# Kernel optimization log

Hardware: AMD Instinct MI355X
Metric: run time of the kernel (lower is better)

The kernel has to match this reference:

```python
import jax, jax.numpy as jnp
import numpy as np

C_CURV = 0.01
K = 20
BALL_EPS = 4e-3  # hyptorch float32 boundary eps


def _e2p(x, c=C_CURV):
    # ToPoincare: expmap0 then project onto the Poincare ball
    sqrt_c = c ** 0.5
    n = jnp.maximum(jnp.linalg.norm(x, axis=-1, keepdims=True), 1e-15)
    y = jnp.tanh(sqrt_c * n) * x / (sqrt_c * n)
    maxnorm = (1.0 - BALL_EPS) / sqrt_c
    ny = jnp.maximum(jnp.linalg.norm(y, axis=-1, keepdims=True), 1e-15)
    return jnp.where(ny > maxnorm, y * (maxnorm / ny), y)


def _mobius_add(x, y, c=C_CURV):
    x2 = jnp.sum(x * x, axis=-1, keepdims=True)
    y2 = jnp.sum(y * y, axis=-1, keepdims=True)
    xy = jnp.sum(x * y, axis=-1, keepdims=True)
    num = (1.0 + 2.0 * c * xy + c * y2) * x + (1.0 - c * x2) * y
    den = 1.0 + 2.0 * c * xy + c * c * x2 * y2
    return num / jnp.maximum(den, 1e-15)


def _knn(x, k):
    # x: (B, C, N); Euclidean negative squared distance, topk indices
    inner = -2.0 * jnp.einsum('bcn,bcm->bnm', x, x)
    xx = jnp.sum(x * x, axis=1)  # (B, N)
    pd = -xx[:, :, None] - inner - xx[:, None, :]
    return jax.lax.top_k(pd, k)[1]  # (B, N, k)


def _graph_feature(x, k=K):
    # x: (B, C, N) -> (B, 2C, N, k)
    idx = _knn(x, k)
    xp = _e2p(jnp.transpose(x, (0, 2, 1)))  # (B, N, C) on Poincare ball
    feat = jax.vmap(lambda xb, ib: xb[ib])(xp, idx)  # (B, N, k, C) gather
    xc = jnp.broadcast_to(xp[:, :, None, :], feat.shape)
    out = jnp.concatenate([_mobius_add(feat, -xc), xc], axis=-1)
    return jnp.transpose(out, (0, 3, 1, 2))


def _bn(x, g, b, axes, eps=1e-5):
    # BatchNorm (training-mode batch statistics), channel axis = 1
    m = jnp.mean(x, axis=axes, keepdims=True)
    v = jnp.mean((x - m) ** 2, axis=axes, keepdims=True)
    shp = [1] * x.ndim
    shp[1] = -1
    return (x - m) / jnp.sqrt(v + eps) * g.reshape(shp) + b.reshape(shp)


def _ln(x, g, b, eps=1e-5):
    m = jnp.mean(x, axis=-1, keepdims=True)
    v = jnp.mean((x - m) ** 2, axis=-1, keepdims=True)
    return (x - m) / jnp.sqrt(v + eps) * g + b


def setup_inputs() -> dict:
    key = jax.random.key(0)
    ks = jax.random.split(key, 8)
    B, N, OUT = 16, 1024, 40
    s = 0.05
    return {
        'x': jax.random.normal(ks[0], (B, N, 3), jnp.float32),
        'conv1_w': jax.random.normal(ks[1], (64, 6), jnp.float32) * s,
        'bn1_g': jnp.ones((64,), jnp.float32), 'bn1_b': jnp.zeros((64,), jnp.float32),
        'conv2_w': jax.random.normal(ks[2], (192, 128), jnp.float32) * s,
        'bn2_g': jnp.ones((192,), jnp.float32), 'bn2_b': jnp.zeros((192,), jnp.float32),
        'conv3_w': jax.random.normal(ks[3], (1024, 256), jnp.float32) * s,
        'bn3_g': jnp.ones((1024,), jnp.float32), 'bn3_b': jnp.zeros((1024,), jnp.float32),
        'fc1_w': jax.random.normal(ks[4], (512, 1024), jnp.float32) * s,
        'fc1_b': jnp.zeros((512,), jnp.float32),
        'ln1_g': jnp.ones((512,), jnp.float32), 'ln1_b': jnp.zeros((512,), jnp.float32),
        'fc2_w': jax.random.normal(ks[5], (256, 512), jnp.float32) * s,
        'fc2_b': jnp.zeros((256,), jnp.float32),
        'ln2_g': jnp.ones((256,), jnp.float32), 'ln2_b': jnp.zeros((256,), jnp.float32),
        'out_w': jax.random.normal(ks[6], (OUT, 256), jnp.float32) * s,
        'out_b': jnp.zeros((OUT,), jnp.float32),
    }


def reference(x, conv1_w, bn1_g, bn1_b, conv2_w, bn2_g, bn2_b,
              conv3_w, bn3_g, bn3_b, fc1_w, fc1_b, ln1_g, ln1_b,
              fc2_w, fc2_b, ln2_g, ln2_b, out_w, out_b):
    xt = jnp.transpose(x, (0, 2, 1))  # (B, 3, N)
    f = _graph_feature(xt)            # (B, 6, N, k)
    h = jnp.einsum('oc,bcnk->bonk', conv1_w, f)
    h = jax.nn.relu(_bn(h, bn1_g, bn1_b, (0, 2, 3)))
    x1 = jnp.max(h, axis=-1)          # (B, 64, N)
    f = _graph_feature(x1)            # (B, 128, N, k)
    h = jnp.einsum('oc,bcnk->bonk', conv2_w, f)
    h = jax.nn.relu(_bn(h, bn2_g, bn2_b, (0, 2, 3)))
    x2 = jnp.max(h, axis=-1)          # (B, 192, N)
    h = jnp.concatenate([x1, x2], axis=1)  # (B, 256, N)
    h = jnp.einsum('oc,bcn->bon', conv3_w, h)
    h = jax.nn.relu(_bn(h, bn3_g, bn3_b, (0, 2)))
    h = jnp.max(h, axis=-1)           # (B, 1024)
    h = jax.nn.relu(_ln(h @ fc1_w.T + fc1_b, ln1_g, ln1_b))
    h = jax.nn.relu(_ln(h @ fc2_w.T + fc2_b, ln2_g, ln2_b))
    logits = h @ out_w.T + out_b      # (B, outdim)
    return jax.nn.log_softmax(logits, axis=1)
```

## Files before the change

kernel.cpp:

```cpp
#include <hip/hip_runtime.h>
#include <math.h>

#define B_ 16
#define N_ 1024
#define KNN 20
#define NPAIR (B_*N_)

typedef __attribute__((ext_vector_type(8))) short bf16x8;
typedef __attribute__((ext_vector_type(4))) float f32x4;

__device__ __forceinline__ unsigned fkey(float f) {
  unsigned u = __float_as_uint(f);
  return (u & 0x80000000u) ? ~u : (u | 0x80000000u);
}
__device__ __forceinline__ float fkeyinv(unsigned u) {
  unsigned b = (u & 0x80000000u) ? (u ^ 0x80000000u) : ~u;
  return __uint_as_float(b);
}
__device__ __forceinline__ unsigned short f2bf(float x) {
  unsigned u = __float_as_uint(x);
  unsigned r = (u + 0x7FFFu + ((u >> 16) & 1u)) >> 16;
  return (unsigned short)r;
}
__device__ __forceinline__ float bf2f(unsigned short u) {
  return __uint_as_float(((unsigned)u) << 16);
}
__device__ __forceinline__ unsigned short f2h(float x) {
  _Float16 h = (_Float16)x;
  return *(unsigned short*)&h;
}
__device__ __forceinline__ float h2f(unsigned short u) {
  _Float16 h = *(_Float16*)&u;
  return (float)h;
}
__device__ __forceinline__ unsigned knnkey(float d, int idx) {
  return (fkey(d) & 0xFFFFFC00u) | (unsigned)(1023 - idx);
}

__device__ __forceinline__ void topk_insert_u32(unsigned (&kl)[KNN], unsigned nk) {
  kl[KNN-1] = nk;
  #pragma unroll
  for (int i = KNN-1; i > 0; i--) {
    unsigned hi = max(kl[i-1], kl[i]);
    unsigned lo = min(kl[i-1], kl[i]);
    kl[i-1] = hi; kl[i] = lo;
  }
}

__device__ __forceinline__ int cnt_gt(const unsigned* __restrict__ L, unsigned v) {
  int j = 0;
  #pragma unroll
  for (int s = 16; s; s >>= 1) {
    int nj = j + s;
    if (nj <= KNN && L[nj-1] > v) j = nj;
  }
  return j;
}

__global__ void __launch_bounds__(256) k_prep_knn1(const float* __restrict__ x,
        float* __restrict__ xp1, const float* __restrict__ w2, const float* __restrict__ w3,
        unsigned short* __restrict__ w2h, unsigned short* __restrict__ wt3h,
        unsigned* __restrict__ keypart) {
  __shared__ float P[N_*3];
  __shared__ float XX[N_];
  if (blockIdx.x >= 512) {
    int i = (blockIdx.x - 512) * 256 + threadIdx.x;
    if (i < NPAIR) {
      float a0 = x[i*3+0], a1 = x[i*3+1], a2 = x[i*3+2];
      float n = sqrtf(a0*a0 + a1*a1 + a2*a2);
      n = fmaxf(n, 1e-15f);
      float th = tanhf(0.1f * n);
      float sc = th / (0.1f * n);
      float ny = fmaxf(th * 10.0f, 1e-15f);
      float mxn = (1.0f - 4e-3f) / 0.1f;
      if (ny > mxn) sc *= mxn / ny;
      xp1[i*3+0] = sc*a0; xp1[i*3+1] = sc*a1; xp1[i*3+2] = sc*a2;
    }
    if (i < 192*128) w2h[i] = f2bf(w2[i]);
    wt3h[i] = f2bf(w3[i]);
    return;
  }
  int blk = blockIdx.x;
  int b = blk >> 5, rc = (blk >> 3) & 3, cc = blk & 7;
  const float* xb = x + b*N_*3;
  for (int e = threadIdx.x; e < N_*3; e += 256) P[e] = xb[e];
  __syncthreads();
  for (int j = threadIdx.x; j < N_; j += 256) {
    float q0 = P[j*3], q1 = P[j*3+1], q2 = P[j*3+2];
    XX[j] = q0*q0 + q1*q1 + q2*q2;
  }
  __syncthreads();
  int r = rc*256 + threadIdx.x;
  float q0 = P[r*3], q1 = P[r*3+1], q2 = P[r*3+2];
  float xxq = XX[r];
  unsigned kl[KNN];
  #pragma unroll
  for (int i = 0; i < KNN; i++) kl[i] = 0u;
  int cbase = cc*128;
  for (int jj = 0; jj < 128; jj++) {
    int j = cbase + jj;
    float dot = q0*P[j*3] + q1*P[j*3+1] + q2*P[j*3+2];
    float d = 2.0f*dot - xxq - XX[j];
    unsigned nk = knnkey(d, j);
    if (nk > kl[KNN-1]) topk_insert_u32(kl, nk);
  }
  int p = b*N_ + r;
  unsigned* pe = keypart + (size_t)p*160 + cc*20;
  #pragma unroll
  for (int i = 0; i < KNN; i++) pe[i] = kl[i];
}

__global__ void __launch_bounds__(256) k_conv1(const float* __restrict__ xp1,
                        const unsigned* __restrict__ keypart,
                        const float* __restrict__ w1, float* __restrict__ hmax1,
                        float* __restrict__ hmin1, float* __restrict__ stats1sh) {
  __shared__ float F[4][KNN][6];
  __shared__ float red[4][64][2];
  __shared__ int idxs[16][KNN];
  __shared__ unsigned keybuf[2560];
  __shared__ unsigned out1[1280];
  __shared__ unsigned out2[640];
  int g = threadIdx.x >> 6, lane = threadIdx.x & 63;
  int tid = threadIdx.x;
  int pbase = blockIdx.x * 16;
  {
    const unsigned* src = keypart + (size_t)pbase*160;
    for (int e = tid; e < 2560; e += 256) keybuf[e] = src[e];
  }
  float w[6];
  #pragma unroll
  for (int c = 0; c < 6; c++) w[c] = w1[lane*6 + c];
  __syncthreads();
  for (int e = tid; e < 2560; e += 256) {
    int pt = e / 160, rem = e - pt*160;
    int m = rem / 40, i = rem - m*40;
    const unsigned* A = keybuf + pt*160 + (2*m)*20;
    const unsigned* Bl = A + 20;
    unsigned v; const unsigned* S; int own;
    if (i < 20) { v = A[i]; S = Bl; own = i; }
    else { v = Bl[i-20]; S = A; own = i-20; }
    int rank = own + cnt_gt(S, v);
    if (rank < KNN) out1[(pt*4 + m)*20 + rank] = v;
  }
  __syncthreads();
  for (int e = tid; e < 1280; e += 256) {
    int pt = e / 80, rem = e - pt*80;
    int m2 = rem / 40, i = rem - m2*40;
    const unsigned* A = out1 + (pt*4 + 2*m2)*20;
    const unsigned* Bl = A + 20;
    unsigned v; const unsigned* S; int own;
    if (i < 20) { v = A[i]; S = Bl; own = i; }
    else { v = Bl[i-20]; S = A; own = i-20; }
    int rank = own + cnt_gt(S, v);
    if (rank < KNN) out2[(pt*2 + m2)*20 + rank] = v;
  }
  __syncthreads();
  for (int e = tid; e < 640; e += 256) {
    int pt = e / 40, i = e - pt*40;
    const unsigned* A = out2 + pt*40;
    const unsigned* Bl = A + 20;
    unsigned v; const unsigned* S; int own;
    if (i < 20) { v = A[i]; S = Bl; own = i; }
    else { v = Bl[i-20]; S = A; own = i-20; }
    int rank = own + cnt_gt(S, v);
    if (rank < KNN) idxs[pt][rank] = 1023 - (int)(v & 1023u);
  }
  float sum = 0.f, sumsq = 0.f;
  __syncthreads();
  for (int it = 0; it < 4; ++it) {
    int p = pbase + it*4 + g;
    if (lane < KNN) {
      int nb = idxs[it*4 + g][lane];
      int bb = p >> 10;
      const float* xc = xp1 + p*3;
      const float* ft = xp1 + (bb*N_ + nb)*3;
      float x0 = ft[0], x1 = ft[1], x2v = ft[2];
      float c0 = xc[0], c1 = xc[1], c2 = xc[2];
      float X2 = x0*x0 + x1*x1 + x2v*x2v;
      float Y2 = c0*c0 + c1*c1 + c2*c2;
      float XY = -(x0*c0 + x1*c1 + x2v*c2);
      float den = fmaxf(1.0f + 0.02f*XY + 1e-4f*X2*Y2, 1e-15f);
      float s1 = (1.0f + 0.02f*XY + 0.01f*Y2) / den;
      float s2 = (1.0f - 0.01f*X2) / den;
      F[g][lane][0] = s1*x0 - s2*c0;
      F[g][lane][1] = s1*x1 - s2*c1;
      F[g][lane][2] = s1*x2v - s2*c2;
      F[g][lane][3] = c0; F[g][lane][4] = c1; F[g][lane][5] = c2;
    }
    __syncthreads();
    float mx = -__builtin_inff(), mn = __builtin_inff();
    for (int k = 0; k < KNN; k++) {
      float h = 0.f;
      #pragma unroll
      for (int c = 0; c < 6; c++) h = fmaf(w[c], F[g][k][c], h);
      mx = fmaxf(mx, h); mn = fminf(mn, h);
      sum += h; sumsq += h*h;
    }
    hmax1[(pbase + it*4 + g)*64 + lane] = mx;
    hmin1[(pbase + it*4 + g)*64 + lane] = mn;
    __syncthreads();
  }
  red[g][lane][0] = sum; red[g][lane][1] = sumsq;
  __syncthreads();
  if (g == 0) {
    float s  = red[0][lane][0] + red[1][lane][0] + red[2][lane][0] + red[3][lane][0];
    float s2 = red[0][lane][1] + red[1][lane][1] + red[2][lane][1] + red[3][lane][1];
    float* dst = stats1sh + ((size_t)(blockIdx.x & 63)*64 + lane)*2;
    atomicAdd(dst, s);
    atomicAdd(dst + 1, s2);
  }
}

__global__ void __launch_bounds__(64) k_bn_reduce(const float* __restrict__ sh, int nch, int nslots,
                            double cnt,
                            const float* __restrict__ g, const float* __restrict__ bb,
                            float* __restrict__ scale, float* __restrict__ shift) {
  int o = blockIdx.x, t = threadIdx.x;
  double s = 0.0, s2 = 0.0;
  for (int sl = t; sl < nslots; sl += 64) {
    s  += (double)sh[((size_t)sl*nch + o)*2];
    s2 += (double)sh[((size_t)sl*nch + o)*2 + 1];
  }
  #pragma unroll
  for (int off = 32; off > 0; off >>= 1) { s += __shfl_xor(s, off); s2 += __shfl_xor(s2, off); }
  if (t == 0) {
    double m = s / cnt;
    double v = s2 / cnt - m*m;
    float a = g[o] / sqrtf((float)v + 1e-5f);
    scale[o] = a;
    shift[o] = bb[o] - a * (float)m;
  }
}

__global__ void __launch_bounds__(256) k_bn1_apply(const float* __restrict__ hmax1, const float* __restrict__ hmin1,
                            const float* __restrict__ scale1, const float* __restrict__ shift1,
                            float* __restrict__ xp2,
                            unsigned short* __restrict__ x1h, unsigned short* __restrict__ x1l,
                            float* __restrict__ xx1) {
  int b = blockIdx.x >> 4, nc = blockIdx.x & 15;
  int c = threadIdx.x & 63, sub = threadIdx.x >> 6;
  int n0 = nc*64 + sub*16;
  float a = scale1[c], t = shift1[c];
  #pragma unroll
  for (int i = 0; i < 16; i++) {
    int p = b*1024 + n0 + i;
    float h = (a >= 0.f) ? hmax1[(size_t)p*64 + c] : hmin1[(size_t)p*64 + c];
    float x1 = fmaxf(fmaf(a, h, t), 0.f);
    unsigned short hb = f2bf(x1);
    x1h[(size_t)p*64 + c] = hb;
    x1l[(size_t)p*64 + c] = f2bf(x1 - bf2f(hb));
    float n2 = x1*x1;
    #pragma unroll
    for (int off = 32; off > 0; off >>= 1) n2 += __shfl_xor(n2, off);
    if (c == 0) xx1[p] = n2;
    float n1 = fmaxf(sqrtf(n2), 1e-15f);
    float th = tanhf(0.1f * n1);
    float sc = th / (0.1f * n1);
    float ny = fmaxf(th * 10.0f, 1e-15f);
    float mxn = (1.0f - 4e-3f) / 0.1f;
    if (ny > mxn) sc *= mxn / ny;
    xp2[(size_t)p*64 + c] = sc * x1;
  }
}

__global__ void __launch_bounds__(256) k_knn2g(const unsigned short* __restrict__ x1h,
        const unsigned short* __restrict__ x1l,
        const float* __restrict__ xx1, unsigned* __restrict__ keypart2) {
  __shared__ __align__(16) float SM[4096];
  int tid = threadIdx.x;
  int bi = blockIdx.x;
  int blk = ((bi & 7) << 7) + (bi >> 3);
  int b = blk >> 6, qc = (blk >> 2) & 15, cc = blk & 3;
  int qbase = qc*64, ccbase = cc*256;
  int wave = tid >> 6, lane = tid & 63;
  int lm = lane & 15, kq = lane >> 4;
  const size_t base = (size_t)b * 65536;

  bf16x8 Qh[4][2], Ql[4][2];
  #pragma unroll
  for (int qt = 0; qt < 4; qt++) {
    size_t ro = base + (size_t)(qbase + qt*16 + lm)*64 + kq*8;
    #pragma unroll
    for (int ks = 0; ks < 2; ks++) {
      Qh[qt][ks] = *((const bf16x8*)(x1h + ro + ks*32));
      Ql[qt][ks] = *((const bf16x8*)(x1l + ro + ks*32));
    }
  }
  unsigned kl[KNN];
  #pragma unroll
  for (int i = 0; i < KNN; i++) kl[i] = 0u;
  int cq = lane + (lane >> 2);

  for (int st = 0; st < 4; ++st) {
    int cb0 = ccbase + st*64;
    size_t co = base + (size_t)(cb0 + wave*16 + lm)*64 + kq*8;
    bf16x8 Ah[2], Al[2];
    #pragma unroll
    for (int ks = 0; ks < 2; ks++) {
      Ah[ks] = *((const bf16x8*)(x1h + co + ks*32));
      Al[ks] = *((const bf16x8*)(x1l + co + ks*32));
    }
    float4 xxc = *((const float4*)(xx1 + b*1024 + cb0 + wave*16 + kq*4));
    f32x4 acc[4];
    #pragma unroll
    for (int qt = 0; qt < 4; qt++) acc[qt] = (f32x4){0.f, 0.f, 0.f, 0.f};
    #pragma unroll
    for (int ks = 0; ks < 2; ks++) {
      #pragma unroll
      for (int qt = 0; qt < 4; qt++) {
        acc[qt] = __builtin_amdgcn_mfma_f32_16x16x32_bf16(Ah[ks], Qh[qt][ks], acc[qt], 0, 0, 0);
        acc[qt] = __builtin_amdgcn_mfma_f32_16x16x32_bf16(Ah[ks], Ql[qt][ks], acc[qt], 0, 0, 0);
        acc[qt] = __builtin_amdgcn_mfma_f32_16x16x32_bf16(Al[ks], Qh[qt][ks], acc[qt], 0, 0, 0);
        acc[qt] = __builtin_amdgcn_mfma_f32_16x16x32_bf16(Al[ks], Ql[qt][ks], acc[qt], 0, 0, 0);
      }
    }
    __syncthreads();
    float xxcv[4] = {xxc.x, xxc.y, xxc.z, xxc.w};
    #pragma unroll
    for (int qt = 0; qt < 4; qt++) {
      int q = qt*16 + lm;
      #pragma unroll
      for (int r = 0; r < 4; r++) {
        int c = wave*16 + kq*4 + r;
        SM[q*64 + ((c + q + (q>>2)) & 63)] = 2.0f*acc[qt][r] - xxcv[r];
      }
    }
    __syncthreads();
    #pragma unroll
    for (int j = 0; j < 16; j++) {
      int c = wave*16 + j;
      float d = SM[lane*64 + ((c + cq) & 63)];
      unsigned nk = knnkey(d, cb0 + c);
      if (nk > kl[KNN-1]) topk_insert_u32(kl, nk);
    }
  }
  __syncthreads();
  unsigned* U = (unsigned*)SM;
  unsigned* L0 = U;
  unsigned* L1 = U + 1344;
  unsigned* M  = U + 2688;
  if (wave == 0) {
    #pragma unroll
    for (int i = 0; i < KNN; i++) L0[lane*21 + i] = kl[i];
  } else if (wave == 1) {
    #pragma unroll
    for (int i = 0; i < KNN; i++) L1[lane*21 + i] = kl[i];
  }
  __syncthreads();
  if (tid < 64) {
    int ia = 0, ib = 0;
    for (int t = 0; t < KNN; t++) {
      unsigned pa = L0[tid*21 + ia], pb = L1[tid*21 + ib];
      bool ta = pa > pb;
      M[tid*21 + t] = ta ? pa : pb;
      if (ta) ia++; else ib++;
    }
  }
  __syncthreads();
  if (wave == 2) {
    #pragma unroll
    for (int i = 0; i < KNN; i++) L0[lane*21 + i] = kl[i];
  } else if (wave == 3) {
    #pragma unroll
    for (int i = 0; i < KNN; i++) L1[lane*21 + i] = kl[i];
  }
  __syncthreads();
  if (tid < 64) {
    int p = b*N_ + qbase + tid;
    unsigned* pe = keypart2 + (size_t)p*80 + cc*20;
    int ia = 0, ib = 0, im = 0;
    for (int t = 0; t < KNN; t++) {
      unsigned pa = L0[tid*21 + ia], pb = L1[tid*21 + ib], pm = M[tid*21 + im];
      unsigned bp = pm; int sel = 2;
      if (pa > bp) { bp = pa; sel = 0; }
      if (pb > bp) { bp = pb; sel = 1; }
      pe[t] = bp;
      if (sel == 0) ia++; else if (sel == 1) ib++; else im++;
    }
  }
}

__global__ void __launch_bounds__(256) k_conv2m(const float* __restrict__ xp2,
    const unsigned* __restrict__ keypart2, const unsigned short* __restrict__ w2h,
    unsigned short* __restrict__ hmax2, unsigned short* __restrict__ hmin2,
    float* __restrict__ stats2sh) {
  __shared__ __align__(16) short Abf[80*136];
  __shared__ __align__(16) float Cf[4][64];
  __shared__ float Yc[4];
  __shared__ int nbr[80];
  __shared__ unsigned keybuf[320];
  int tid = threadIdx.x;
  int bi = blockIdx.x;
  int g512 = ((bi & 7) << 9) + (bi >> 3);
  int p0 = g512 * 4;
  int b = p0 >> 10;
  for (int e = tid; e < 320; e += 256) keybuf[e] = keypart2[(size_t)p0*80 + e];
  if (tid < 64) {
    int pt = tid >> 4, qq = tid & 15;
    float4 cv = *((const float4*)(xp2 + (size_t)(p0 + pt)*64) + qq);
    *((float4*)&Cf[pt][qq*4]) = cv;
    float y2 = cv.x*cv.x + cv.y*cv.y + cv.z*cv.z + cv.w*cv.w;
    #pragma unroll
    for (int off = 8; off > 0; off >>= 1) y2 += __shfl_xor(y2, off);
    if (qq == 0) Yc[pt] = y2;
    ushort4 cb;
    cb.x = f2bf(cv.x); cb.y = f2bf(cv.y); cb.z = f2bf(cv.z); cb.w = f2bf(cv.w);
    #pragma unroll
    for (int a = 0; a < 5; a++)
      #pragma unroll
      for (int j2 = 0; j2 < 4; j2++)
        *((ushort4*)(Abf + (a*16 + pt*4 + j2)*136 + 64 + qq*4)) = cb;
  }
  __syncthreads();
  for (int e = tid; e < 320; e += 256) {
    int pt = e / 80;
    int rem = e - pt*80;
    int c = rem / 20;
    int i = rem - c*20;
    const unsigned* LB = keybuf + pt*80;
    unsigned v = LB[c*20 + i];
    int rank = i;
    #pragma unroll
    for (int c2 = 0; c2 < 4; c2++) {
      if (c2 == c) continue;
      rank += cnt_gt(LB + c2*20, v);
    }
    if (rank < KNN) nbr[pt*20 + rank] = 1023 - (int)(v & 1023u);
  }
  __syncthreads();
  for (int e = tid; e < 80*16; e += 256) {
    int r = e >> 4, qq = e & 15;
    int q = (r >> 2) & 3;
    int L = 20*q + 4*(r >> 4) + (r & 3);
    float4 f = *((const float4*)(xp2 + (size_t)(b*N_ + nbr[L])*64) + qq);
    float4 cvf = *((const float4*)&Cf[q][qq*4]);
    float X2 = f.x*f.x + f.y*f.y + f.z*f.z + f.w*f.w;
    float XY = -(f.x*cvf.x + f.y*cvf.y + f.z*cvf.z + f.w*cvf.w);
    #pragma unroll
    for (int off = 8; off > 0; off >>= 1) {
      X2 += __shfl_xor(X2, off);
      XY += __shfl_xor(XY, off);
    }
    float Y2 = Yc[q];
    float den = fmaxf(1.0f + 0.02f*XY + 1e-4f*X2*Y2, 1e-15f);
    float inv = 1.0f / den;
    float s1 = (1.0f + 0.02f*XY + 0.01f*Y2) * inv;
    float s2 = (1.0f - 0.01f*X2) * inv;
    ushort4 mo;
    mo.x = f2bf(s1*f.x - s2*cvf.x);
    mo.y = f2bf(s1*f.y - s2*cvf.y);
    mo.z = f2bf(s1*f.z - s2*cvf.z);
    mo.w = f2bf(s1*f.w - s2*cvf.w);
    *((ushort4*)(Abf + r*136 + qq*4)) = mo;
  }
  __syncthreads();
  int wave = tid >> 6, lane = tid & 63;
  int quad = lane >> 4, lm = lane & 15;
  int colbase = wave*48;
  f32x4 acc[5][3];
  #pragma unroll
  for (int rt = 0; rt < 5; rt++)
    #pragma unroll
    for (int cj = 0; cj < 3; cj++) acc[rt][cj] = (f32x4){0.f, 0.f, 0.f, 0.f};
  #pragma unroll
  for (int kt = 0; kt < 4; kt++) {
    int k0 = kt*32 + quad*8;
    bf16x8 bf[3];
    #pragma unroll
    for (int cj = 0; cj < 3; cj++)
      bf[cj] = *((const bf16x8*)(w2h + (size_t)(colbase + cj*16 + lm)*128 + k0));
    bf16x8 af[5];
    #pragma unroll
    for (int rt = 0; rt < 5; rt++)
      af[rt] = *((const bf16x8*)(Abf + (rt*16 + lm)*136 + k0));
    #pragma unroll
    for (int rt = 0; rt < 5; rt++)
      #pragma unroll
      for (int cj = 0; cj < 3; cj++)
        acc[rt][cj] = __builtin_amdgcn_mfma_f32_16x16x32_bf16(af[rt], bf[cj], acc[rt][cj], 0, 0, 0);
  }
  #pragma unroll
  for (int cj = 0; cj < 3; cj++) {
    int o = colbase + cj*16 + lm;
    float s = 0.f, s2 = 0.f, mx = -__builtin_inff(), mn = __builtin_inff();
    #pragma unroll
    for (int rt = 0; rt < 5; rt++) {
      #pragma unroll
      for (int reg = 0; reg < 4; reg++) {
        float h = acc[rt][cj][reg];
        s += h; s2 += h*h;
        mx = fmaxf(mx, h); mn = fminf(mn, h);
      }
    }
    hmax2[(size_t)(p0 + quad)*192 + o] = f2h(mx);
    hmin2[(size_t)(p0 + quad)*192 + o] = f2h(mn);
    s  += __shfl_xor(s, 16);  s  += __shfl_xor(s, 32);
    s2 += __shfl_xor(s2, 16); s2 += __shfl_xor(s2, 32);
    if (lane < 16) {
      float* dst = stats2sh + ((size_t)(bi & 255)*192 + o)*2;
      atomicAdd(dst, s); atomicAdd(dst + 1, s2);
    }
  }
}

__global__ void __launch_bounds__(256) k_conv3m(
   const unsigned short* __restrict__ x1h,
   const unsigned short* __restrict__ hmax2, const unsigned short* __restrict__ hmin2,
   const float* __restrict__ scale2, const float* __restrict__ shift2,
   const unsigned short* __restrict__ wt3h, float* __restrict__ stats3sh,
   unsigned* __restrict__ hmax3u, unsigned* __restrict__ hmin3u) {
  __shared__ short As[64*264];
  int tid = threadIdx.x;
  int mt = blockIdx.x >> 2, cb = blockIdx.x & 3;
  int rowbase = mt*64;
  int b = rowbase >> 10;
  int c4 = tid & 63;
  float4 sc, sh;
  if (c4 >= 16) {
    sc = *((const float4*)(scale2 + (c4*4 - 64)));
    sh = *((const float4*)(shift2 + (c4*4 - 64)));
  }
  #pragma unroll 4
  for (int i = 0; i < 16; i++) {
    int r = (tid >> 6) + i*4;
    int p = rowbase + r;
    if (c4 < 16) {
      *((ushort4*)(As + r*264 + c4*4)) =
        *((const ushort4*)(x1h + (size_t)p*64 + c4*4));
    } else {
      ushort4 hx4 = *((const ushort4*)(hmax2 + (size_t)p*192 + (c4*4 - 64)));
      ushort4 hn4 = *((const ushort4*)(hmin2 + (size_t)p*192 + (c4*4 - 64)));
      ushort4 o4;
      o4.x = f2bf(fmaxf(fmaf(sc.x, (sc.x >= 0.f ? h2f(hx4.x) : h2f(hn4.x)), sh.x), 0.f));
      o4.y = f2bf(fmaxf(fmaf(sc.y, (sc.y >= 0.f ? h2f(hx4.y) : h2f(hn4.y)), sh.y), 0.f));
      o4.z = f2bf(fmaxf(fmaf(sc.z, (sc.z >= 0.f ? h2f(hx4.z) : h2f(hn4.z)), sh.z), 0.f));
      o4.w = f2bf(fmaxf(fmaf(sc.w, (sc.w >= 0.f ? h2f(hx4.w) : h2f(hn4.w)), sh.w), 0.f));
      *((ushort4*)(As + r*264 + c4*4)) = o4;
    }
  }
  __syncthreads();
  int wave = tid >> 6, lane = tid & 63;
  int quad = lane >> 4, lm = lane & 15;
  int colbase = cb*256 + wave*64;
  f32x4 acc[4][4];
  #pragma unroll
  for (int ri = 0; ri < 4; ri++)
    #pragma unroll
    for (int cj = 0; cj < 4; cj++) acc[ri][cj] = (f32x4){0.f, 0.f, 0.f, 0.f};
  for (int kt = 0; kt < 8; kt++) {
    int k0 = kt*32 + quad*8;
    bf16x8 bf[4];
    #pragma unroll
    for (int cj = 0; cj < 4; cj++)
      bf[cj] = *((const bf16x8*)(wt3h + (size_t)(colbase + cj*16 + lm)*256 + k0));
    bf16x8 af[4];
    #pragma unroll
    for (int ri = 0; ri < 4; ri++)
      af[ri] = *((const bf16x8*)(As + (ri*16 + lm)*264 + k0));
    #pragma unroll
    for (int ri = 0; ri < 4; ri++)
      #pragma unroll
      for (int cj = 0; cj < 4; cj++)
        acc[ri][cj] = __builtin_amdgcn_mfma_f32_16x16x32_bf16(af[ri], bf[cj], acc[ri][cj], 0, 0, 0);
  }
  #pragma unroll
  for (int cj = 0; cj < 4; cj++) {
    float s = 0.f, s2 = 0.f, mx = -__builtin_inff(), mn = __builtin_inff();
    #pragma unroll
    for (int ri = 0; ri < 4; ri++) {
      #pragma unroll
      for (int reg = 0; reg < 4; reg++) {
        float h = acc[ri][cj][reg];
        s += h; s2 += h*h; mx = fmaxf(mx, h); mn = fminf(mn, h);
      }
    }
    s  += __shfl_xor(s, 16);  s  += __shfl_xor(s, 32);
    s2 += __shfl_xor(s2, 16); s2 += __shfl_xor(s2, 32);
    mx = fmaxf(mx, __shfl_xor(mx, 16)); mx = fmaxf(mx, __shfl_xor(mx, 32));
    mn = fminf(mn, __shfl_xor(mn, 16)); mn = fminf(mn, __shfl_xor(mn, 32));
    if (lane < 16) {
      int col = colbase + cj*16 + lane;
      float* dst = stats3sh + ((size_t)(blockIdx.x & 63)*1024 + col)*2;
      atomicAdd(dst, s);
      atomicAdd(dst + 1, s2);
      atomicMax(hmax3u + b*1024 + col, fkey(mx));
      atomicMin(hmin3u + b*1024 + col, fkey(mn));
    }
  }
}

__device__ float blk_reduce(float v, float* red, int tid) {
  red[tid] = v; __syncthreads();
  for (int st = 128; st > 0; st >>= 1) {
    if (tid < st) red[tid] += red[tid + st];
    __syncthreads();
  }
  float r = red[0]; __syncthreads();
  return r;
}

__global__ void __launch_bounds__(256) k_head1(const unsigned* __restrict__ hmax3u,
    const unsigned* __restrict__ hmin3u,
    const float* __restrict__ scale3, const float* __restrict__ shift3,
    const float* __restrict__ fc1w, const float* __restrict__ fc1b,
    float* __restrict__ h1buf) {
  __shared__ __align__(16) float V[1024];
  int b = blockIdx.x >> 5, oc = blockIdx.x & 31;
  int tid = threadIdx.x;
  for (int o = tid; o < 1024; o += 256) {
    float a = scale3[o];
    unsigned u = (a >= 0.f) ? hmax3u[b*1024 + o] : hmin3u[b*1024 + o];
    V[o] = fmaxf(fmaf(a, fkeyinv(u), shift3[o]), 0.f);
  }
  __syncthreads();
  int ty = tid >> 4, tx = tid & 15;
  int o = oc*16 + ty;
  const float4* wr = (const float4*)(fc1w + (size_t)o*1024) + tx*16;
  const float4* vv = (const float4*)V + tx*16;
  float s = 0.f;
  #pragma unroll
  for (int i = 0; i < 16; i++) {
    float4 w = wr[i]; float4 v = vv[i];
    s = fmaf(w.x, v.x, s); s = fmaf(w.y, v.y, s);
    s = fmaf(w.z, v.z, s); s = fmaf(w.w, v.w, s);
  }
  s += __shfl_xor(s, 1); s += __shfl_xor(s, 2);
  s += __shfl_xor(s, 4); s += __shfl_xor(s, 8);
  if (tx == 0) h1buf[b*512 + o] = s + fc1b[o];
}

__global__ void __launch_bounds__(256) k_head2(const float* __restrict__ h1buf,
    const float* __restrict__ ln1g, const float* __restrict__ ln1b,
    const float* __restrict__ fc2w, const float* __restrict__ fc2b,
    float* __restrict__ h2buf) {
  __shared__ __align__(16) float H1[512];
  __shared__ float red[256];
  int b = blockIdx.x >> 3, oc = blockIdx.x & 7;
  int tid = threadIdx.x;
  float v0 = h1buf[b*512 + tid], v1 = h1buf[b*512 + 256 + tid];
  float s = blk_reduce(v0 + v1, red, tid);
  float s2 = blk_reduce(v0*v0 + v1*v1, red, tid);
  float m = s / 512.f;
  float var = s2 / 512.f - m*m;
  float inv = 1.0f / sqrtf(var + 1e-5f);
  H1[tid] = fmaxf((v0 - m)*inv*ln1g[tid] + ln1b[tid], 0.f);
  H1[256 + tid] = fmaxf((v1 - m)*inv*ln1g[256 + tid] + ln1b[256 + tid], 0.f);
  __syncthreads();
  int ty = tid >> 3, tx = tid & 7;
  int o = oc*32 + ty;
  const float4* wr = (const float4*)(fc2w + (size_t)o*512) + tx*16;
  const float4* vv = (const float4*)H1 + tx*16;
  float t = 0.f;
  #pragma unroll
  for (int i = 0; i < 16; i++) {
    float4 w = wr[i]; float4 v = vv[i];
    t = fmaf(w.x, v.x, t); t = fmaf(w.y, v.y, t);
    t = fmaf(w.z, v.z, t); t = fmaf(w.w, v.w, t);
  }
  t += __shfl_xor(t, 1); t += __shfl_xor(t, 2); t += __shfl_xor(t, 4);
  if (tx == 0) h2buf[b*256 + o] = t + fc2b[o];
}

__global__ void __launch_bounds__(256) k_head3(const float* __restrict__ h2buf,
    const float* __restrict__ ln2g, const float* __restrict__ ln2b,
    const float* __restrict__ outw, const float* __restrict__ outb,
    float* __restrict__ out) {
  __shared__ __align__(16) float H2[256];
  __shared__ float red[256];
  int b = blockIdx.x, tid = threadIdx.x;
  float h2v = h2buf[b*256 + tid];
  float ss = blk_reduce(h2v, red, tid);
  float ss2 = blk_reduce(h2v*h2v, red, tid);
  float m2 = ss / 256.f;
  float var2 = ss2 / 256.f - m2*m2;
  float inv2 = 1.0f / sqrtf(var2 + 1e-5f);
  H2[tid] = fmaxf((h2v - m2)*inv2*ln2g[tid] + ln2b[tid], 0.f);
  __syncthreads();
  if (tid < 40) {
    const float4* wr = (const float4*)(outw + (size_t)tid*256);
    float t = 0.f;
    for (int c4 = 0; c4 < 64; c4++) {
      float4 w = wr[c4]; float4 vv = ((const float4*)H2)[c4];
      t = fmaf(w.x, vv.x, t); t = fmaf(w.y, vv.y, t);
      t = fmaf(w.z, vv.z, t); t = fmaf(w.w, vv.w, t);
    }
    red[tid] = t + outb[tid];
  }
  __syncthreads();
  if (tid == 0) {
    float mx = -__builtin_inff();
    for (int i2 = 0; i2 < 40; i2++) mx = fmaxf(mx, red[i2]);
    float se = 0.f;
    for (int i2 = 0; i2 < 40; i2++) se += expf(red[i2] - mx);
    float lse = mx + logf(se);
    for (int i2 = 0; i2 < 40; i2++) out[b*40 + i2] = red[i2] - lse;
  }
}

extern "C" void kernel_launch(void* const* d_in, const int* in_sizes, int n_in,
                              void* d_out, int out_size, void* d_ws, size_t ws_size,
                              hipStream_t stream) {
  (void)in_sizes; (void)n_in; (void)out_size; (void)ws_size;
  const float* x    = (const float*)d_in[0];
  const float* w1   = (const float*)d_in[1];
  const float* bn1g = (const float*)d_in[2];
  const float* bn1b = (const float*)d_in[3];
  const float* w2   = (const float*)d_in[4];
  const float* bn2g = (const float*)d_in[5];
  const float* bn2b = (const float*)d_in[6];
  const float* w3   = (const float*)d_in[7];
  const float* bn3g = (const float*)d_in[8];
  const float* bn3b = (const float*)d_in[9];
  const float* fc1w = (const float*)d_in[10];
  const float* fc1b = (const float*)d_in[11];
  const float* ln1g = (const float*)d_in[12];
  const float* ln1b = (const float*)d_in[13];
  const float* fc2w = (const float*)d_in[14];
  const float* fc2b = (const float*)d_in[15];
  const float* ln2g = (const float*)d_in[16];
  const float* ln2b = (const float*)d_in[17];
  const float* outw = (const float*)d_in[18];
  const float* outb = (const float*)d_in[19];
  float* out = (float*)d_out;

  float* ws = (float*)d_ws;
  size_t off = 0;
  float* xp1   = ws + off; off += 49152;
  float* hmax1 = ws + off; off += 1048576;
  float* hmin1 = ws + off; off += 1048576;
  float* xp2   = ws + off; off += 1048576;
  float* hmax2f = ws + off; off += 3145728;
  float* hmin2f = ws + off; off += 3145728;
  unsigned* keypart2 = (unsigned*)(ws + off); off += 1310720;
  unsigned short* w2h = (unsigned short*)(ws + off); off += 24576;
  unsigned short* wt3h = (unsigned short*)(ws + off); off += 131072;
  float* x1bf  = ws + off; off += 1048576;
  float* xx1   = ws + off; off += 16384;
  float* h1buf = ws + off; off += 8192;
  float* h2buf = ws + off; off += 4096;
  float* scale1 = ws + off; off += 64;
  float* shift1 = ws + off; off += 64;
  float* scale2 = ws + off; off += 192;
  float* shift2 = ws + off; off += 192;
  float* scale3 = ws + off; off += 1024;
  float* shift3 = ws + off; off += 1024;
  float* stats1sh = ws + off;
  float* stats2sh = stats1sh + 64*64*2;
  float* stats3sh = stats2sh + (size_t)256*192*2;
  unsigned* hmax3u = (unsigned*)(stats3sh + (size_t)64*1024*2);
  unsigned* hmin3u = hmax3u + 16384;
  unsigned* keypartA = (unsigned*)hmax2f;
  unsigned short* x1h = (unsigned short*)x1bf;
  unsigned short* x1l = x1h + 1048576;
  unsigned short* hmax2 = (unsigned short*)hmax2f;
  unsigned short* hmin2 = (unsigned short*)hmin2f;

  size_t zero_bytes = ((size_t)64*64*2 + (size_t)256*192*2 + (size_t)64*1024*2)*4 + (size_t)16384*4;
  hipMemsetAsync(stats1sh, 0, zero_bytes, stream);
  hipMemsetAsync(hmin3u, 0xFF, (size_t)16384*4, stream);

  k_prep_knn1<<<1536, 256, 0, stream>>>(x, xp1, w2, w3, w2h, wt3h, keypartA);
  k_conv1<<<1024, 256, 0, stream>>>(xp1, keypartA, w1, hmax1, hmin1, stats1sh);
  k_bn_reduce<<<64, 64, 0, stream>>>(stats1sh, 64, 64, 327680.0, bn1g, bn1b, scale1, shift1);
  k_bn1_apply<<<256, 256, 0, stream>>>(hmax1, hmin1, scale1, shift1, xp2, x1h, x1l, xx1);
  k_knn2g<<<1024, 256, 0, stream>>>(x1h, x1l, xx1, keypart2);
  k_conv2m<<<4096, 256, 0, stream>>>(xp2, keypart2, w2h, hmax2, hmin2, stats2sh);
  k_bn_reduce<<<192, 64, 0, stream>>>(stats2sh, 192, 256, 327680.0, bn2g, bn2b, scale2, shift2);
  k_conv3m<<<1024, 256, 0, stream>>>(x1h, hmax2, hmin2, scale2, shift2,
                                     wt3h, stats3sh, hmax3u, hmin3u);
  k_bn_reduce<<<1024, 64, 0, stream>>>(stats3sh, 1024, 64, 16384.0, bn3g, bn3b, scale3, shift3);
  k_head1<<<512, 256, 0, stream>>>(hmax3u, hmin3u, scale3, shift3, fc1w, fc1b, h1buf);
  k_head2<<<128, 256, 0, stream>>>(h1buf, ln1g, ln1b, fc2w, fc2b, h2buf);
  k_head3<<<16, 256, 0, stream>>>(h2buf, ln2g, ln2b, outw, outb, out);
}
```

Baseline: 345.7 us.

## Use per-wave LDS scratch in knn2 and parallel rank-based top-k merge

Each wave now writes its distance tile to a private padded LDS region (stride 17), which removes the two block-wide barriers per candidate stage. The serial single-wave merge of the four per-wave top-k lists is replaced by a parallel merge-by-rank: every thread takes one element, counts the larger elements in the other list to find its output position, and does this in two rounds using all 256 threads. LDS usage grows because a separate 5376-word buffer is added, and correctness relies on cnt_gt and on the keys being distinct.

```diff
diff --git a/kernel.cpp b/kernel.cpp
--- a/kernel.cpp
+++ b/kernel.cpp
@@ -266,7 +266,8 @@
 __global__ void __launch_bounds__(256) k_knn2g(const unsigned short* __restrict__ x1h,
         const unsigned short* __restrict__ x1l,
         const float* __restrict__ xx1, unsigned* __restrict__ keypart2) {
-  __shared__ __align__(16) float SM[4096];
+  __shared__ __align__(16) float SLC[4352];
+  __shared__ unsigned LU[5376];
   int tid = threadIdx.x;
   int bi = blockIdx.x;
   int blk = ((bi & 7) << 7) + (bi >> 3);
@@ -275,6 +276,7 @@
   int wave = tid >> 6, lane = tid & 63;
   int lm = lane & 15, kq = lane >> 4;
   const size_t base = (size_t)b * 65536;
+  float* SW = SLC + wave*1088;
 
   bf16x8 Qh[4][2], Ql[4][2];
   #pragma unroll
@@ -289,7 +291,6 @@
   unsigned kl[KNN];
   #pragma unroll
   for (int i = 0; i < KNN; i++) kl[i] = 0u;
-  int cq = lane + (lane >> 2);
 
   for (int st = 0; st < 4; ++st) {
     int cb0 = ccbase + st*64;
@@ -314,69 +315,48 @@
         acc[qt] = __builtin_amdgcn_mfma_f32_16x16x32_bf16(Al[ks], Ql[qt][ks], acc[qt], 0, 0, 0);
       }
     }
-    __syncthreads();
     float xxcv[4] = {xxc.x, xxc.y, xxc.z, xxc.w};
     #pragma unroll
     for (int qt = 0; qt < 4; qt++) {
       int q = qt*16 + lm;
       #pragma unroll
       for (int r = 0; r < 4; r++) {
-        int c = wave*16 + kq*4 + r;
-        SM[q*64 + ((c + q + (q>>2)) & 63)] = 2.0f*acc[qt][r] - xxcv[r];
+        SW[q*17 + kq*4 + r] = 2.0f*acc[qt][r] - xxcv[r];
       }
     }
-    __syncthreads();
     #pragma unroll
     for (int j = 0; j < 16; j++) {
-      int c = wave*16 + j;
-      float d = SM[lane*64 + ((c + cq) & 63)];
-      unsigned nk = knnkey(d, cb0 + c);
+      float d = SW[lane*17 + j];
+      unsigned nk = knnkey(d, cb0 + wave*16 + j);
       if (nk > kl[KNN-1]) topk_insert_u32(kl, nk);
     }
   }
-  __syncthreads();
-  unsigned* U = (unsigned*)SM;
-  unsigned* L0 = U;
-  unsigned* L1 = U + 1344;
-  unsigned* M  = U + 2688;
-  if (wave == 0) {
-    #pragma unroll
-    for (int i = 0; i < KNN; i++) L0[lane*21 + i] = kl[i];
-  } else if (wave == 1) {
-    #pragma unroll
-    for (int i = 0; i < KNN; i++) L1[lane*21 + i] = kl[i];
-  }
-  __syncthreads();
-  if (tid < 64) {
-    int ia = 0, ib = 0;
-    for (int t = 0; t < KNN; t++) {
-      unsigned pa = L0[tid*21 + ia], pb = L1[tid*21 + ib];
-      bool ta = pa > pb;
-      M[tid*21 + t] = ta ? pa : pb;
-      if (ta) ia++; else ib++;
-    }
-  }
-  __syncthreads();
-  if (wave == 2) {
-    #pragma unroll
-    for (int i = 0; i < KNN; i++) L0[lane*21 + i] = kl[i];
-  } else if (wave == 3) {
-    #pragma unroll
-    for (int i = 0; i < KNN; i++) L1[lane*21 + i] = kl[i];
-  }
-  __syncthreads();
-  if (tid < 64) {
-    int p = b*N_ + qbase + tid;
-    unsigned* pe = keypart2 + (size_t)p*80 + cc*20;
-    int ia = 0, ib = 0, im = 0;
-    for (int t = 0; t < KNN; t++) {
-      unsigned pa = L0[tid*21 + ia], pb = L1[tid*21 + ib], pm = M[tid*21 + im];
-      unsigned bp = pm; int sel = 2;
-      if (pa > bp) { bp = pa; sel = 0; }
-      if (pb > bp) { bp = pb; sel = 1; }
-      pe[t] = bp;
-      if (sel == 0) ia++; else if (sel == 1) ib++; else im++;
-    }
+  #pragma unroll
+  for (int i = 0; i < KNN; i++) LU[wave*1344 + lane*21 + i] = kl[i];
+  __syncthreads();
+  unsigned* MU = (unsigned*)SLC;
+  for (int e = tid; e < 5120; e += 256) {
+    int pair = e / 2560;
+    int rem = e - pair*2560;
+    int q = rem / 40;
+    int i40 = rem - q*40;
+    int side = (i40 >= 20) ? 1 : 0;
+    int idx = i40 - side*20;
+    int own = pair*2 + side, oth = pair*2 + (1 - side);
+    unsigned v = LU[own*1344 + q*21 + idx];
+    int rank = idx + cnt_gt(LU + oth*1344 + q*21, v);
+    if (rank < KNN) MU[pair*1344 + q*21 + rank] = v;
+  }
+  __syncthreads();
+  for (int e = tid; e < 2560; e += 256) {
+    int q = e / 40;
+    int i40 = e - q*40;
+    int side = (i40 >= 20) ? 1 : 0;
+    int idx = i40 - side*20;
+    unsigned v = MU[side*1344 + q*21 + idx];
+    int rank = idx + cnt_gt(MU + (1 - side)*1344 + q*21, v);
+    if (rank < KNN)
+      keypart2[(size_t)(b*N_ + qbase + q)*80 + cc*20 + rank] = v;
   }
 }
 
```

New measurement: 350.0 us. About the same (+1.2%).
